# Performance work log

Measured on AMD Instinct MI355X. Metric: run time of the kernel, lower is better.

## Reference

```python
import jax, jax.numpy as jnp
import numpy as np

D_MODEL = 128; NS = 8; D_FF = 512; N_CROSS = 3; N_SELF = 2; PRED = 4
B = 2; N = 5; Q = 2500; HF = 24; WF = 77
VX, VY, VZ = 32, 16, 32  # voxel grid (x, y, z); volume layout [B, C, VY, VX, VZ]


def grid_sample_2d(feat, grid):
    # feat [B,C,H,W]; grid [B,*S,2] xy in [-1,1]; bilinear, align_corners=True, zeros padding
    Bf, C, H, W = feat.shape
    gs = grid.shape[1:-1]
    g = grid.reshape(Bf, -1, 2)
    x = (g[..., 0] + 1.0) * 0.5 * (W - 1)
    y = (g[..., 1] + 1.0) * 0.5 * (H - 1)
    x0 = jnp.floor(x); y0 = jnp.floor(y)
    xd = x - x0; yd = y - y0
    featf = feat.reshape(Bf, C, H * W)
    def corner(xi, yi, w8):
        valid = (xi >= 0) & (xi < W) & (yi >= 0) & (yi < H)
        idx = jnp.clip(yi, 0, H - 1).astype(jnp.int32) * W + jnp.clip(xi, 0, W - 1).astype(jnp.int32)
        gathered = jnp.take_along_axis(featf, idx[:, None, :], axis=2)  # [B,C,P]
        return gathered * (w8 * valid)[:, None, :]
    out = (corner(x0, y0, (1 - xd) * (1 - yd)) + corner(x0 + 1, y0, xd * (1 - yd))
           + corner(x0, y0 + 1, (1 - xd) * yd) + corner(x0 + 1, y0 + 1, xd * yd))
    return out.reshape(Bf, C, *gs)


def grid_sample_3d(feat, grid):
    # feat [B,C,D,H,W]; grid [B,*S,3] with channels (x->W, y->H, z->D); zeros padding
    Bf, C, D, H, W = feat.shape
    gs = grid.shape[1:-1]
    g = grid.reshape(Bf, -1, 3)
    x = (g[..., 0] + 1.0) * 0.5 * (W - 1)
    y = (g[..., 1] + 1.0) * 0.5 * (H - 1)
    z = (g[..., 2] + 1.0) * 0.5 * (D - 1)
    x0 = jnp.floor(x); y0 = jnp.floor(y); z0 = jnp.floor(z)
    xd = x - x0; yd = y - y0; zd = z - z0
    featf = feat.reshape(Bf, C, D * H * W)
    def corner(xi, yi, zi, w8):
        valid = (xi >= 0) & (xi < W) & (yi >= 0) & (yi < H) & (zi >= 0) & (zi < D)
        idx = (jnp.clip(zi, 0, D - 1).astype(jnp.int32) * (H * W)
               + jnp.clip(yi, 0, H - 1).astype(jnp.int32) * W
               + jnp.clip(xi, 0, W - 1).astype(jnp.int32))
        gathered = jnp.take_along_axis(featf, idx[:, None, :], axis=2)
        return gathered * (w8 * valid)[:, None, :]
    out = (corner(x0, y0, z0, (1 - xd) * (1 - yd) * (1 - zd))
           + corner(x0 + 1, y0, z0, xd * (1 - yd) * (1 - zd))
           + corner(x0, y0 + 1, z0, (1 - xd) * yd * (1 - zd))
           + corner(x0 + 1, y0 + 1, z0, xd * yd * (1 - zd))
           + corner(x0, y0, z0 + 1, (1 - xd) * (1 - yd) * zd)
           + corner(x0 + 1, y0, z0 + 1, xd * (1 - yd) * zd)
           + corner(x0, y0 + 1, z0 + 1, (1 - xd) * yd * zd)
           + corner(x0 + 1, y0 + 1, z0 + 1, xd * yd * zd))
    return out.reshape(Bf, C, *gs)


def layer_norm(x, g, b):
    mu = x.mean(-1, keepdims=True)
    var = ((x - mu) ** 2).mean(-1, keepdims=True)
    return (x - mu) / jnp.sqrt(var + 1e-5) * g + b


def setup_inputs() -> dict:
    key = jax.random.key(0)
    ks = iter(jax.random.split(key, 64))
    def rn(shape, scale=0.02):
        return (jax.random.normal(next(ks), shape) * scale).astype(jnp.float32)
    inp = {
        'query': jax.random.normal(next(ks), (B, Q, D_MODEL), jnp.float32),
        'ref_points': jax.random.uniform(next(ks), (B, N, Q, 2), jnp.float32),
        'ref_points_3d': jax.random.uniform(next(ks), (B, Q, 3), jnp.float32) * 2.0 - 1.0,
        'image_features': jax.random.normal(next(ks), (B * N, D_MODEL, HF, WF), jnp.float32),
        'mask': jax.random.randint(next(ks), (B, N, Q), 0, 2) > 0,
        'x_idx': jax.random.randint(next(ks), (B, Q), 0, VX, dtype=jnp.int32),
        'y_idx': jax.random.randint(next(ks), (B, Q), 0, VY, dtype=jnp.int32),
        'z_idx': jax.random.randint(next(ks), (B, Q), 0, VZ, dtype=jnp.int32),
        # cross-attn layers (stacked over N_CROSS)
        'c_ln1_g': jnp.ones((N_CROSS, D_MODEL), jnp.float32), 'c_ln1_b': jnp.zeros((N_CROSS, D_MODEL), jnp.float32),
        'c_dp_w': rn((N_CROSS, D_MODEL, NS * 2)), 'c_dp_b': jnp.zeros((N_CROSS, NS * 2), jnp.float32),
        'c_a_w': rn((N_CROSS, D_MODEL, NS)), 'c_a_b': jnp.zeros((N_CROSS, NS), jnp.float32),
        'c_w_w': rn((N_CROSS, D_MODEL, D_MODEL)), 'c_w_b': jnp.zeros((N_CROSS, D_MODEL), jnp.float32),
        'c_vp_w': rn((N_CROSS, D_MODEL, D_MODEL)), 'c_vp_b': jnp.zeros((N_CROSS, D_MODEL), jnp.float32),
        'c_op_w': rn((N_CROSS, D_MODEL, D_MODEL)), 'c_op_b': jnp.zeros((N_CROSS, D_MODEL), jnp.float32),
        'c_ln2_g': jnp.ones((N_CROSS, D_MODEL), jnp.float32), 'c_ln2_b': jnp.zeros((N_CROSS, D_MODEL), jnp.float32),
        'c_ff1_w': rn((N_CROSS, D_MODEL, D_FF)), 'c_ff1_b': jnp.zeros((N_CROSS, D_FF), jnp.float32),
        'c_ff2_w': rn((N_CROSS, D_FF, D_MODEL)), 'c_ff2_b': jnp.zeros((N_CROSS, D_MODEL), jnp.float32),
        # self-attn layers (stacked over N_SELF)
        's_ln1_g': jnp.ones((N_SELF, D_MODEL), jnp.float32), 's_ln1_b': jnp.zeros((N_SELF, D_MODEL), jnp.float32),
        's_dp_w': rn((N_SELF, D_MODEL, NS * 3)), 's_dp_b': jnp.zeros((N_SELF, NS * 3), jnp.float32),
        's_a_w': rn((N_SELF, D_MODEL, NS)), 's_a_b': jnp.zeros((N_SELF, NS), jnp.float32),
        's_w_w': rn((N_SELF, D_MODEL, D_MODEL)), 's_w_b': jnp.zeros((N_SELF, D_MODEL), jnp.float32),
        's_vp_w': rn((N_SELF, D_MODEL, D_MODEL)), 's_vp_b': jnp.zeros((N_SELF, D_MODEL), jnp.float32),
        's_op_w': rn((N_SELF, D_MODEL, D_MODEL)), 's_op_b': jnp.zeros((N_SELF, D_MODEL), jnp.float32),
        's_ln2_g': jnp.ones((N_SELF, D_MODEL), jnp.float32), 's_ln2_b': jnp.zeros((N_SELF, D_MODEL), jnp.float32),
        's_ff1_w': rn((N_SELF, D_MODEL, D_FF)), 's_ff1_b': jnp.zeros((N_SELF, D_FF), jnp.float32),
        's_ff2_w': rn((N_SELF, D_FF, D_MODEL)), 's_ff2_b': jnp.zeros((N_SELF, D_MODEL), jnp.float32),
        'cls_w': rn((D_MODEL, PRED)), 'cls_b': jnp.zeros((PRED,), jnp.float32),
    }
    return inp


def reference(query, ref_points, ref_points_3d, image_features, mask, x_idx, y_idx, z_idx,
              c_ln1_g, c_ln1_b, c_dp_w, c_dp_b, c_a_w, c_a_b, c_w_w, c_w_b, c_vp_w, c_vp_b,
              c_op_w, c_op_b, c_ln2_g, c_ln2_b, c_ff1_w, c_ff1_b, c_ff2_w, c_ff2_b,
              s_ln1_g, s_ln1_b, s_dp_w, s_dp_b, s_a_w, s_a_b, s_w_w, s_w_b, s_vp_w, s_vp_b,
              s_op_w, s_op_b, s_ln2_g, s_ln2_b, s_ff1_w, s_ff1_b, s_ff2_w, s_ff2_b, cls_w, cls_b):
    mf = mask.astype(query.dtype)  # [B,N,Q]
    flat_idx = y_idx * (VX * VZ) + x_idx * VZ + z_idx  # [B,Q], vol layout [B,C,VY,VX,VZ]
    bb = jnp.arange(B)[:, None]

    # ---- deformable cross attention stack ----
    for i in range(N_CROSS):
        q_ln = layer_norm(query, c_ln1_g[i], c_ln1_b[i])
        dp = (q_ln @ c_dp_w[i] + c_dp_b[i]).reshape(B, Q, NS, 2)
        pd = (ref_points[:, :, :, None, :] + dp[:, None]) * 2.0 - 1.0  # [B,N,Q,Ns,2]
        vf = jnp.einsum('bchw,cd->bdhw', image_features, c_vp_w[i]) + c_vp_b[i][None, :, None, None]
        samp = grid_sample_2d(vf, pd.reshape(B * N, Q, NS, 2))  # [B*N,C,Q,Ns]
        samp = samp.reshape(B, N, D_MODEL, Q, NS).transpose(0, 1, 3, 4, 2)  # [B,N,Q,Ns,C]
        wf = samp @ c_w_w[i] + c_w_b[i]
        att = jax.nn.softmax(q_ln @ c_a_w[i] + c_a_b[i], axis=-1)  # [B,Q,Ns]
        s = (wf * att[:, None, :, :, None]).sum(3)  # [B,N,Q,C]
        s = (s * mf[..., None]).sum(1) / (mf.sum(1)[..., None] + 1e-6)  # masked mean over cameras
        query = query + (s @ c_op_w[i] + c_op_b[i])
        h = layer_norm(query, c_ln2_g[i], c_ln2_b[i])
        h = jax.nn.gelu(h @ c_ff1_w[i] + c_ff1_b[i], approximate=False) @ c_ff2_w[i] + c_ff2_b[i]
        query = query + h

    # ---- voxel scatter + deformable self attention stack ----
    m_any = jnp.any(mask, axis=1).astype(query.dtype)  # [B,Q]
    for i in range(N_SELF):
        vol = jnp.zeros((B, VY * VX * VZ, D_MODEL), query.dtype).at[bb, flat_idx].set(query)
        vol = vol.reshape(B, VY, VX, VZ, D_MODEL).transpose(0, 4, 1, 2, 3)  # [B,C,16,32,32]
        q_ln = layer_norm(query, s_ln1_g[i], s_ln1_b[i])
        dp = (q_ln @ s_dp_w[i] + s_dp_b[i]).reshape(B, Q, NS, 3)
        pd = ref_points_3d[:, :, None, :] + dp
        pd = pd[..., jnp.array([1, 0, 2])]  # permute coords as in torch code
        samp = grid_sample_3d(vol, pd)  # [B,C,Q,Ns]
        samp = samp.transpose(0, 2, 3, 1)  # [B,Q,Ns,C]
        v = samp @ s_vp_w[i] + s_vp_b[i]
        wf = v @ s_w_w[i] + s_w_b[i]
        att = jax.nn.softmax(q_ln @ s_a_w[i] + s_a_b[i], axis=-1)
        s = (wf * att[..., None]).sum(2)  # [B,Q,C]
        s = s * m_any[..., None]
        query = query + (s @ s_op_w[i] + s_op_b[i])
        h = layer_norm(query, s_ln2_g[i], s_ln2_b[i])
        h = jax.nn.gelu(h @ s_ff1_w[i] + s_ff1_b[i], approximate=False) @ s_ff2_w[i] + s_ff2_b[i]
        query = query + h

    logits = query @ cls_w + cls_b  # [B,Q,pred_num]
    return logits
```

## Files before the change

kernel.cpp:

```cpp
#include <hip/hip_runtime.h>
#include <math.h>

#define D_MODELC 128
#define NSAMP 8
#define DFF 512
#define NCROSS 3
#define NSELF 2
#define BB 2
#define NCAM 5
#define QQ 2500
#define HFI 24
#define WFI 77
#define VXC 32
#define VYC 16
#define VZC 32
#define BQ (BB*QQ)
#define HWI (HFI*WFI)
#define NVOX (VYC*VXC*VZC)

typedef float f4 __attribute__((ext_vector_type(4)));
typedef short s8v __attribute__((ext_vector_type(8)));

__device__ __forceinline__ unsigned short f2bf(float f) {
  union { float f; unsigned u; } v; v.f = f;
  unsigned r = v.u + 0x7FFFu + ((v.u >> 16) & 1u);
  return (unsigned short)(r >> 16);
}
__device__ __forceinline__ float bf2f(unsigned short u) {
  union { unsigned u; float f; } v; v.u = ((unsigned)u) << 16; return v.f;
}

__device__ __forceinline__ bool mask_at(const unsigned char* m, int fl, int idx) {
  if (fl) return m[idx] != 0;
  return ((const int*)m)[idx] != 0;
}

__global__ __launch_bounds__(1024) void mask_k(const unsigned char* __restrict__ m,
                                               int* __restrict__ flag,
                                               float* __restrict__ invden, float* __restrict__ imc,
                                               float* __restrict__ many) {
  __shared__ int f;
  if (threadIdx.x == 0) f = 0;
  __syncthreads();
  const int total = BB * NCAM * QQ;
  int loc = 0;
  for (int i = threadIdx.x; i < total; i += 1024)
    if ((i & 3) && m[i]) loc = 1;
  if (loc) atomicOr(&f, 1);
  __syncthreads();
  int fl = f;
  if (threadIdx.x == 0) *flag = fl;
  for (int i = threadIdx.x; i < BQ; i += 1024) {
    int b = i / QQ, q = i % QQ;
    float cnt = 0.f;
    for (int n = 0; n < NCAM; ++n)
      cnt += mask_at(m, fl, (b * NCAM + n) * QQ + q) ? 1.f : 0.f;
    float inv = 1.f / (cnt + 1e-6f);
    invden[i] = inv;
    imc[i] = cnt * inv;
    many[i] = cnt > 0.f ? 1.f : 0.f;
  }
}

__global__ __launch_bounds__(256) void transpose_img_k(const float* __restrict__ in,
                                                       unsigned short* __restrict__ out) {
  __shared__ float til[32][65];
  int bn = blockIdx.z;
  int c0 = blockIdx.y * 32;
  int yx0 = blockIdx.x * 64;
  int t = threadIdx.x;
  {
    int yx_l = t & 63, c_l = t >> 6;
    int yx = yx0 + yx_l;
#pragma unroll
    for (int i = 0; i < 8; ++i) {
      int c = c_l + 4 * i;
      float v = 0.f;
      if (yx < HWI) v = in[((size_t)(bn * D_MODELC + c0 + c)) * HWI + yx];
      til[c][yx_l] = v;
    }
  }
  __syncthreads();
  {
    int yx_l = t >> 2, cc = (t & 3) * 8;
    int yx = yx0 + yx_l;
    if (yx < HWI) {
      union { unsigned short u[8]; s8v v; } pk;
#pragma unroll
      for (int j = 0; j < 8; ++j) pk.u[j] = f2bf(til[cc + j][yx_l]);
      *(s8v*)(out + ((size_t)bn * HWI + yx) * D_MODELC + c0 + cc) = pk.v;
    }
  }
}

__global__ __launch_bounds__(256) void zero_vol_k(unsigned short* __restrict__ vol,
                                                  int* __restrict__ winner) {
  int idx = blockIdx.x * 256 + threadIdx.x;
  const int nv16 = (BB * NVOX * 128) / 8;
  if (idx < nv16) {
    uint4 z = make_uint4(0, 0, 0, 0);
    *(uint4*)(vol + (size_t)idx * 8) = z;
  }
  const int nw4 = (BB * NVOX) / 4;
  if (idx < nw4) {
    int4 m = make_int4(-1, -1, -1, -1);
    *(int4*)(winner + (size_t)idx * 4) = m;
  }
}

__global__ void scatter_winner_k(const int* __restrict__ xi, const int* __restrict__ yi,
                                 const int* __restrict__ zi, int* __restrict__ winner) {
  int i = blockIdx.x * blockDim.x + threadIdx.x;
  if (i >= BQ) return;
  int b = i / QQ;
  int vox = yi[i] * (VXC * VZC) + xi[i] * VZC + zi[i];
  atomicMax(&winner[b * NVOX + vox], i % QQ);
}

__global__ void scatter_write_k(const int* __restrict__ xi, const int* __restrict__ yi,
                                const int* __restrict__ zi, const int* __restrict__ winner,
                                const float* __restrict__ qb, unsigned short* __restrict__ vol) {
  int idx = blockIdx.x * blockDim.x + threadIdx.x;
  if (idx >= BQ * 16) return;
  int g = idx & 15, row = idx >> 4;
  int b = row / QQ, q = row % QQ;
  int vox = yi[row] * (VXC * VZC) + xi[row] * VZC + zi[row];
  if (winner[b * NVOX + vox] != q) return;
  const float* src = qb + (size_t)row * 128 + g * 8;
  float4 a = *(const float4*)src;
  float4 c = *(const float4*)(src + 4);
  union { unsigned short u[8]; s8v v; } pk;
  pk.u[0] = f2bf(a.x); pk.u[1] = f2bf(a.y); pk.u[2] = f2bf(a.z); pk.u[3] = f2bf(a.w);
  pk.u[4] = f2bf(c.x); pk.u[5] = f2bf(c.y); pk.u[6] = f2bf(c.z); pk.u[7] = f2bf(c.w);
  *(s8v*)(vol + ((size_t)b * NVOX + vox) * 128 + g * 8) = pk.v;
}

__global__ __launch_bounds__(256) void tpre_k(const float* __restrict__ c_w_w, const float* __restrict__ s_w_w,
                                              const float* __restrict__ c_op_w, const float* __restrict__ s_op_w,
                                              const float* __restrict__ cf1, const float* __restrict__ sf1,
                                              const float* __restrict__ cf2, const float* __restrict__ sf2,
                                              float* __restrict__ Qbuf,
                                              unsigned short* __restrict__ f1T, unsigned short* __restrict__ f2T) {
  __shared__ float As_[32][64];
  __shared__ float Ws_[32][64];
  int z = blockIdx.z, tid = threadIdx.x;
  if (z < 5) {
    const float* A = (z < 3) ? c_w_w + (size_t)z * 16384 : s_w_w + (size_t)(z - 3) * 16384;
    const float* Bm = (z < 3) ? c_op_w + (size_t)z * 16384 : s_op_w + (size_t)(z - 3) * 16384;
    float* C = Qbuf + (size_t)z * 16384;
    int m0 = blockIdx.x * 64, n0 = blockIdx.y * 64;
    float acc[4][4] = {};
    int mr = (tid >> 4) * 4, nc = (tid & 15) * 4;
    for (int k0 = 0; k0 < 128; k0 += 32) {
      {
        int r = tid >> 2, kq = (tid & 3) * 8;
        const float* ap = A + (size_t)(m0 + r) * 128 + k0 + kq;
        float4 v0 = *(const float4*)ap, v1 = *(const float4*)(ap + 4);
        As_[kq + 0][r] = v0.x; As_[kq + 1][r] = v0.y; As_[kq + 2][r] = v0.z; As_[kq + 3][r] = v0.w;
        As_[kq + 4][r] = v1.x; As_[kq + 5][r] = v1.y; As_[kq + 6][r] = v1.z; As_[kq + 7][r] = v1.w;
      }
      {
        int kr = tid >> 3, nq = (tid & 7) * 8;
        const float* wp = Bm + (size_t)(k0 + kr) * 128 + n0 + nq;
        *(float4*)&Ws_[kr][nq] = *(const float4*)wp;
        *(float4*)&Ws_[kr][nq + 4] = *(const float4*)(wp + 4);
      }
      __syncthreads();
#pragma unroll
      for (int kk = 0; kk < 32; ++kk) {
        float4 av = *(const float4*)&As_[kk][mr];
        float4 bv = *(const float4*)&Ws_[kk][nc];
        float a_[4] = {av.x, av.y, av.z, av.w};
        float b_[4] = {bv.x, bv.y, bv.z, bv.w};
#pragma unroll
        for (int i = 0; i < 4; ++i)
#pragma unroll
          for (int j = 0; j < 4; ++j) acc[i][j] += a_[i] * b_[j];
      }
      __syncthreads();
    }
#pragma unroll
    for (int i = 0; i < 4; ++i) {
      float4 r;
      r.x = acc[i][0]; r.y = acc[i][1]; r.z = acc[i][2]; r.w = acc[i][3];
      *(float4*)(C + (size_t)(m0 + mr + i) * 128 + n0 + nc) = r;
    }
  } else {
    int bid = (z - 5) * 4 + blockIdx.y * 2 + blockIdx.x;
    int widx = bid >> 6, chunk = bid & 63;
    const float* src; unsigned short* dst; int K, N;
    if (widx < 5) {
      src = (widx < 3) ? cf1 + (size_t)widx * 65536 : sf1 + (size_t)(widx - 3) * 65536;
      dst = f1T + (size_t)widx * 65536; K = 128; N = 512;
    } else {
      int L = widx - 5;
      src = (L < 3) ? cf2 + (size_t)L * 65536 : sf2 + (size_t)(L - 3) * 65536;
      dst = f2T + (size_t)L * 65536; K = 512; N = 128;
    }
    int e = (chunk * 256 + tid) * 4;
    int k = e % K, n = e / K;
    ushort4 o;
    o.x = f2bf(src[(size_t)(k + 0) * N + n]);
    o.y = f2bf(src[(size_t)(k + 1) * N + n]);
    o.z = f2bf(src[(size_t)(k + 2) * N + n]);
    o.w = f2bf(src[(size_t)(k + 3) * N + n]);
    *(ushort4*)(dst + e) = o;
  }
}

struct P5 { const float* a[5]; const float* b[5]; float* c[5]; };

__global__ __launch_bounds__(256) void small_mm_k(P5 ps) {
  const float* A = ps.a[blockIdx.z];
  const float* Bm = ps.b[blockIdx.z];
  float* C = ps.c[blockIdx.z];
  __shared__ float As_[32][64];
  __shared__ float Ws_[32][64];
  int m0 = blockIdx.x * 64, n0 = blockIdx.y * 64, tid = threadIdx.x;
  float acc[4][4] = {};
  int mr = (tid >> 4) * 4, nc = (tid & 15) * 4;
  for (int k0 = 0; k0 < 128; k0 += 32) {
    {
      int r = tid >> 2, kq = (tid & 3) * 8;
      const float* ap = A + (size_t)(m0 + r) * 128 + k0 + kq;
      float4 v0 = *(const float4*)ap, v1 = *(const float4*)(ap + 4);
      As_[kq + 0][r] = v0.x; As_[kq + 1][r] = v0.y; As_[kq + 2][r] = v0.z; As_[kq + 3][r] = v0.w;
      As_[kq + 4][r] = v1.x; As_[kq + 5][r] = v1.y; As_[kq + 6][r] = v1.z; As_[kq + 7][r] = v1.w;
    }
    {
      int kr = tid >> 3, nq = (tid & 7) * 8;
      const float* wp = Bm + (size_t)(k0 + kr) * 128 + n0 + nq;
      *(float4*)&Ws_[kr][nq] = *(const float4*)wp;
      *(float4*)&Ws_[kr][nq + 4] = *(const float4*)(wp + 4);
    }
    __syncthreads();
#pragma unroll
    for (int kk = 0; kk < 32; ++kk) {
      float4 av = *(const float4*)&As_[kk][mr];
      float4 bv = *(const float4*)&Ws_[kk][nc];
      float a_[4] = {av.x, av.y, av.z, av.w};
      float b_[4] = {bv.x, bv.y, bv.z, bv.w};
#pragma unroll
      for (int i = 0; i < 4; ++i)
#pragma unroll
        for (int j = 0; j < 4; ++j) acc[i][j] += a_[i] * b_[j];
    }
    __syncthreads();
  }
#pragma unroll
  for (int i = 0; i < 4; ++i) {
    float4 r;
    r.x = acc[i][0]; r.y = acc[i][1]; r.z = acc[i][2]; r.w = acc[i][3];
    *(float4*)(C + (size_t)(m0 + mr + i) * 128 + n0 + nc) = r;
  }
}

__global__ __launch_bounds__(256) void wpre_k(const float* __restrict__ Wcbuf,
                                              unsigned short* __restrict__ WcT,
                                              const float* __restrict__ c_vp_b, const float* __restrict__ c_w_b,
                                              const float* __restrict__ s_vp_b, const float* __restrict__ s_w_b,
                                              const float* __restrict__ c_op_w, const float* __restrict__ s_op_w,
                                              const float* __restrict__ Qbuf,
                                              float* __restrict__ v1buf, float* __restrict__ v2buf,
                                              float* __restrict__ csbuf) {
  int t = threadIdx.x;
  if (blockIdx.y < 5) {
    int L = blockIdx.y;
    const float* src = Wcbuf + (size_t)L * 16384;
    unsigned short* dst = WcT + (size_t)L * 16384;
    int e = (blockIdx.x * 256 + t) * 4;
    int k = e & 127, n = e >> 7;
    ushort4 o;
    o.x = f2bf(src[(size_t)(k + 0) * 128 + n]);
    o.y = f2bf(src[(size_t)(k + 1) * 128 + n]);
    o.z = f2bf(src[(size_t)(k + 2) * 128 + n]);
    o.w = f2bf(src[(size_t)(k + 3) * 128 + n]);
    *(ushort4*)(dst + e) = o;
  } else if (blockIdx.x < 5 && t < 128) {
    int L = blockIdx.x, n = t;
    const float* vpb = L < 3 ? c_vp_b + L * 128 : s_vp_b + (L - 3) * 128;
    const float* wb = L < 3 ? c_w_b + L * 128 : s_w_b + (L - 3) * 128;
    const float* op = L < 3 ? c_op_w + (size_t)L * 16384 : s_op_w + (size_t)(L - 3) * 16384;
    const float* Q = Qbuf + (size_t)L * 16384;
    float a = 0.f, c = 0.f;
    for (int k = 0; k < 128; ++k) {
      a += vpb[k] * Q[k * 128 + n];
      c += wb[k] * op[k * 128 + n];
    }
    if (L < 3) { v1buf[L * 128 + n] = a; v2buf[L * 128 + n] = c; }
    else csbuf[(L - 3) * 128 + n] = a + c;
  }
}

__global__ __launch_bounds__(512) void cross_mega_k(
    const float* __restrict__ query, const float* __restrict__ refp,
    const unsigned char* __restrict__ maskp, const int* __restrict__ flagp,
    const float* __restrict__ invden, const float* __restrict__ imc,
    const unsigned short* __restrict__ imgT,
    const float* __restrict__ ln1g, const float* __restrict__ ln1b,
    const float* __restrict__ dpw_, const float* __restrict__ dpb_,
    const float* __restrict__ aw_, const float* __restrict__ ab_,
    const unsigned short* __restrict__ WcT, const float* __restrict__ opb_,
    const float* __restrict__ v1_, const float* __restrict__ v2_,
    const float* __restrict__ ln2g, const float* __restrict__ ln2b,
    const unsigned short* __restrict__ f1T, const float* __restrict__ b1_,
    const unsigned short* __restrict__ f2T, const float* __restrict__ b2_,
    float* __restrict__ qb) {
  __shared__ float qtile[8][136];
  __shared__ float pr[8][24];
  __shared__ float awa[8];
  __shared__ __align__(16) unsigned short As[16 * 128];
  __shared__ __align__(16) char scratch[16896];
  int* soff = (int*)scratch;
  float* sw = (float*)(scratch + 5120);
  float* wl = (float*)scratch;
  unsigned short* Hs = (unsigned short*)scratch;

  int t = threadIdx.x;
  int m0 = blockIdx.x * 8;
  int wv = t >> 6, lane = t & 63;
  int la = lane & 15, lb = lane >> 4;
  int fl = *flagp;
  if (lane < 32)
    *(float4*)&qtile[wv][lane * 4] = *(const float4*)(query + (size_t)(m0 + wv) * 128 + lane * 4);
  if (t < 128) {
    s8v z = {};
    *(s8v*)&As[(8 + (t >> 4)) * 128 + (t & 15) * 8] = z;
  }
  __syncthreads();

  for (int L = 0; L < NCROSS; ++L) {
    const float* dpw = dpw_ + (size_t)L * 2048;
    const float* dpb = dpb_ + L * 16;
    const float* aw = aw_ + (size_t)L * 1024;
    const float* ab = ab_ + L * 8;
    const float* g1 = ln1g + L * 128;
    const float* be1 = ln1b + L * 128;
    for (int idx = t; idx < 24 * 128; idx += 512) {
      int c = idx >> 7, k = idx & 127;
      wl[c * 132 + k] = (c < 16) ? dpw[k * 16 + c] : aw[k * 8 + (c - 16)];
    }
    __syncthreads();
    {
      int c0 = lane * 2;
      float x0 = qtile[wv][c0], x1 = qtile[wv][c0 + 1];
      float s1 = x0 + x1, s2 = x0 * x0 + x1 * x1;
#pragma unroll
      for (int msk = 1; msk < 64; msk <<= 1) { s1 += __shfl_xor(s1, msk); s2 += __shfl_xor(s2, msk); }
      float mean = s1 * (1.f / 128.f);
      float var = s2 * (1.f / 128.f) - mean * mean;
      float inv = rsqrtf(var + 1e-5f);
      float l0 = (x0 - mean) * inv * g1[c0] + be1[c0];
      float l1 = (x1 - mean) * inv * g1[c0 + 1] + be1[c0 + 1];
      float p[24];
#pragma unroll
      for (int c = 0; c < 24; ++c)
        p[c] = l0 * wl[c * 132 + c0] + l1 * wl[c * 132 + c0 + 1];
#pragma unroll
      for (int msk = 1; msk < 64; msk <<= 1) {
#pragma unroll
        for (int c = 0; c < 24; ++c) p[c] += __shfl_xor(p[c], msk);
      }
      if (lane == 0) {
#pragma unroll
        for (int c = 0; c < 24; ++c) pr[wv][c] = p[c];
      }
    }
    __syncthreads();
    if (t < 320) {
      int qi = t / 40, rem = t % 40;
      int n = rem >> 3, s = rem & 7;
      int row = m0 + qi;
      int b = row / QQ, q = row - b * QQ;
      int mi = (b * NCAM + n) * QQ + q;
      bool mk = mask_at(maskp, fl, mi);
      float mx = -1e30f;
      float av[8];
#pragma unroll
      for (int i = 0; i < 8; ++i) { av[i] = pr[qi][16 + i] + ab[i]; mx = fmaxf(mx, av[i]); }
      float sm = 0.f, es = 0.f;
#pragma unroll
      for (int i = 0; i < 8; ++i) {
        float e_ = expf(av[i] - mx);
        sm += e_;
        if (i == s) es = e_;
      }
      float a = mk ? es / sm : 0.f;
      float rx = refp[(size_t)mi * 2 + 0];
      float ry = refp[(size_t)mi * 2 + 1];
      float fx = (rx + pr[qi][s * 2 + 0] + dpb[s * 2 + 0]) * (float)(WFI - 1);
      float fy = (ry + pr[qi][s * 2 + 1] + dpb[s * 2 + 1]) * (float)(HFI - 1);
      float x0f = floorf(fx), y0f = floorf(fy);
      int x0 = (int)x0f, y0 = (int)y0f;
      float xd = fx - x0f, yd = fy - y0f;
      int base = (b * NCAM + n) * HWI;
#pragma unroll
      for (int cy = 0; cy < 2; ++cy)
#pragma unroll
        for (int cx = 0; cx < 2; ++cx) {
          int xi = x0 + cx, yi = y0 + cy;
          bool ok = (xi >= 0) & (xi < WFI) & (yi >= 0) & (yi < HFI);
          int xc = min(max(xi, 0), WFI - 1), yc = min(max(yi, 0), HFI - 1);
          soff[t * 4 + cy * 2 + cx] = (base + yc * WFI + xc) * 128;
          sw[t * 4 + cy * 2 + cx] = ok ? a * (cx ? xd : 1.f - xd) * (cy ? yd : 1.f - yd) : 0.f;
        }
    }
    __syncthreads();
    {
      int qi = wv, ln = lane & 15, eg = lane >> 4;
      float acc[8] = {};
      float wa = 0.f;
      for (int e = eg * 10; e < eg * 10 + 10; ++e) {
        int eb = qi * 40 + e;
        float4 wv4 = *(const float4*)&sw[eb * 4];
        int4 ov = *(const int4*)&soff[eb * 4];
        s8v p0 = *(const s8v*)(imgT + (size_t)ov.x + ln * 8);
        s8v p1 = *(const s8v*)(imgT + (size_t)ov.y + ln * 8);
        s8v p2 = *(const s8v*)(imgT + (size_t)ov.z + ln * 8);
        s8v p3 = *(const s8v*)(imgT + (size_t)ov.w + ln * 8);
#pragma unroll
        for (int i = 0; i < 8; ++i)
          acc[i] += wv4.x * bf2f((unsigned short)p0[i]) + wv4.y * bf2f((unsigned short)p1[i])
                  + wv4.z * bf2f((unsigned short)p2[i]) + wv4.w * bf2f((unsigned short)p3[i]);
        wa += wv4.x + wv4.y + wv4.z + wv4.w;
      }
#pragma unroll
      for (int i = 0; i < 8; ++i) { acc[i] += __shfl_xor(acc[i], 16); acc[i] += __shfl_xor(acc[i], 32); }
      wa += __shfl_xor(wa, 16); wa += __shfl_xor(wa, 32);
      if (eg == 0) {
        union { unsigned short u[8]; s8v v; } pk;
#pragma unroll
        for (int i = 0; i < 8; ++i) pk.u[i] = f2bf(acc[i]);
        *(s8v*)&As[qi * 128 + ((ln ^ (qi & 7)) << 3)] = pk.v;
        if (ln == 0) awa[qi] = wa;
      }
    }
    __syncthreads();
    {
      const unsigned short* Wc = WcT + (size_t)L * 16384;
      const float* v1L = v1_ + L * 128;
      const float* v2L = v2_ + L * 128;
      const float* opbL = opb_ + L * 128;
      f4 accm = {};
      int col = wv * 16 + la;
#pragma unroll
      for (int ks = 0; ks < 4; ++ks) {
        s8v af = *(const s8v*)&As[la * 128 + (((ks * 4 + lb) ^ (la & 7)) << 3)];
        s8v bf = *(const s8v*)(Wc + (size_t)col * 128 + ks * 32 + lb * 8);
        accm = __builtin_amdgcn_mfma_f32_16x16x32_bf16(af, bf, accm, 0, 0, 0);
      }
#pragma unroll
      for (int j = 0; j < 4; ++j) {
        int lr = lb * 4 + j;
        if (lr < 8) {
          int m = m0 + lr;
          float s0m = invden[m];
          qtile[lr][col] += accm[j] * s0m + s0m * awa[lr] * v1L[col] + imc[m] * v2L[col] + opbL[col];
        }
      }
    }
    __syncthreads();
    {
      const float* g2 = ln2g + L * 128;
      const float* be2 = ln2b + L * 128;
      int c0 = lane * 2;
      float x0 = qtile[wv][c0], x1 = qtile[wv][c0 + 1];
      float s1 = x0 + x1, s2 = x0 * x0 + x1 * x1;
#pragma unroll
      for (int msk = 1; msk < 64; msk <<= 1) { s1 += __shfl_xor(s1, msk); s2 += __shfl_xor(s2, msk); }
      float mean = s1 * (1.f / 128.f);
      float var = s2 * (1.f / 128.f) - mean * mean;
      float inv = rsqrtf(var + 1e-5f);
      unsigned u0 = f2bf((x0 - mean) * inv * g2[c0] + be2[c0]);
      unsigned u1 = f2bf((x1 - mean) * inv * g2[c0 + 1] + be2[c0 + 1]);
      int chunk = lane >> 2, idx2 = (lane & 3) * 2;
      *(unsigned*)&As[wv * 128 + ((chunk ^ (wv & 7)) << 3) + idx2] = u0 | (u1 << 16);
    }
    __syncthreads();
    {
      const unsigned short* W1 = f1T + (size_t)L * 65536;
      const float* b1 = b1_ + L * 512;
      f4 acc1[4] = {};
#pragma unroll
      for (int ks = 0; ks < 4; ++ks) {
        s8v af = *(const s8v*)&As[la * 128 + (((ks * 4 + lb) ^ (la & 7)) << 3)];
#pragma unroll
        for (int ti = 0; ti < 4; ++ti) {
          int col = (wv * 4 + ti) * 16 + la;
          s8v bf = *(const s8v*)(W1 + (size_t)col * 128 + ks * 32 + lb * 8);
          acc1[ti] = __builtin_amdgcn_mfma_f32_16x16x32_bf16(af, bf, acc1[ti], 0, 0, 0);
        }
      }
#pragma unroll
      for (int ti = 0; ti < 4; ++ti) {
        int col = (wv * 4 + ti) * 16 + la;
        int chunk = col >> 3, idx = col & 7;
#pragma unroll
        for (int j = 0; j < 4; ++j) {
          int m = lb * 4 + j;
          float val = 0.f;
          if (m < 8) {
            val = acc1[ti][j] + b1[col];
            val = 0.5f * val * (1.f + erff(val * 0.70710678118654752f));
          }
          Hs[m * 512 + ((chunk ^ (m & 7)) << 3) + idx] = f2bf(val);
        }
      }
    }
    __syncthreads();
    {
      const unsigned short* W2 = f2T + (size_t)L * 65536;
      const float* b2 = b2_ + L * 128;
      f4 acc2 = {};
      int col = wv * 16 + la;
#pragma unroll
      for (int ks = 0; ks < 16; ++ks) {
        s8v af = *(const s8v*)&Hs[la * 512 + (((ks * 4 + lb) ^ (la & 7)) << 3)];
        s8v bf = *(const s8v*)(W2 + (size_t)col * 512 + ks * 32 + lb * 8);
        acc2 = __builtin_amdgcn_mfma_f32_16x16x32_bf16(af, bf, acc2, 0, 0, 0);
      }
#pragma unroll
      for (int j = 0; j < 4; ++j) {
        int lr = lb * 4 + j;
        if (lr < 8) qtile[lr][col] += acc2[j] + b2[col];
      }
    }
    __syncthreads();
  }
  if (lane < 32)
    *(float4*)(qb + (size_t)(m0 + wv) * 128 + lane * 4) = *(const float4*)&qtile[wv][lane * 4];
}

template <bool CLS>
__global__ __launch_bounds__(512) void self_mega_k(
    const float* __restrict__ qbin, const float* __restrict__ ref3d,
    const unsigned short* __restrict__ vol, const float* __restrict__ many,
    const float* __restrict__ ln1g, const float* __restrict__ ln1b,
    const float* __restrict__ dpw, const float* __restrict__ dpb,
    const float* __restrict__ aw, const float* __restrict__ ab,
    const unsigned short* __restrict__ WcT, const float* __restrict__ opb,
    const float* __restrict__ csb,
    const float* __restrict__ ln2g, const float* __restrict__ ln2b,
    const unsigned short* __restrict__ f1T, const float* __restrict__ b1,
    const unsigned short* __restrict__ f2T, const float* __restrict__ b2,
    float* __restrict__ qb,
    const float* __restrict__ cw, const float* __restrict__ cb, float* __restrict__ out) {
  __shared__ float qtile[8][136];
  __shared__ float pr[8][32];
  __shared__ __align__(16) unsigned short As[16 * 128];
  __shared__ __align__(16) char scratch[16896];
  int* soff = (int*)scratch;
  float* sw = (float*)(scratch + 2048);
  float* wl = (float*)scratch;
  unsigned short* Hs = (unsigned short*)scratch;

  int t = threadIdx.x;
  int m0 = blockIdx.x * 8;
  int wv = t >> 6, lane = t & 63;
  int la = lane & 15, lb = lane >> 4;
  if (lane < 32)
    *(float4*)&qtile[wv][lane * 4] = *(const float4*)(qbin + (size_t)(m0 + wv) * 128 + lane * 4);
  if (t < 128) {
    s8v z = {};
    *(s8v*)&As[(8 + (t >> 4)) * 128 + (t & 15) * 8] = z;
  }
  for (int idx = t; idx < 32 * 128; idx += 512) {
    int c = idx >> 7, k = idx & 127;
    wl[c * 132 + k] = (c < 24) ? dpw[k * 24 + c] : aw[k * 8 + (c - 24)];
  }
  __syncthreads();
  {
    int c0 = lane * 2;
    float x0 = qtile[wv][c0], x1 = qtile[wv][c0 + 1];
    float s1 = x0 + x1, s2 = x0 * x0 + x1 * x1;
#pragma unroll
    for (int msk = 1; msk < 64; msk <<= 1) { s1 += __shfl_xor(s1, msk); s2 += __shfl_xor(s2, msk); }
    float mean = s1 * (1.f / 128.f);
    float var = s2 * (1.f / 128.f) - mean * mean;
    float inv = rsqrtf(var + 1e-5f);
    float l0 = (x0 - mean) * inv * ln1g[c0] + ln1b[c0];
    float l1 = (x1 - mean) * inv * ln1g[c0 + 1] + ln1b[c0 + 1];
    float p[32];
#pragma unroll
    for (int c = 0; c < 32; ++c)
      p[c] = l0 * wl[c * 132 + c0] + l1 * wl[c * 132 + c0 + 1];
#pragma unroll
    for (int msk = 1; msk < 64; msk <<= 1) {
#pragma unroll
      for (int c = 0; c < 32; ++c) p[c] += __shfl_xor(p[c], msk);
    }
    if (lane == 0) {
#pragma unroll
      for (int c = 0; c < 32; ++c) pr[wv][c] = p[c];
    }
  }
  __syncthreads();
  if (t < 64) {
    int qi = t >> 3, s = t & 7;
    int row = m0 + qi;
    int b = row / QQ;
    float mx = -1e30f;
    float av[8];
#pragma unroll
    for (int i = 0; i < 8; ++i) { av[i] = pr[qi][24 + i] + ab[i]; mx = fmaxf(mx, av[i]); }
    float sm = 0.f, es = 0.f;
#pragma unroll
    for (int i = 0; i < 8; ++i) {
      float e_ = expf(av[i] - mx);
      sm += e_;
      if (i == s) es = e_;
    }
    float a = es / sm;
    float g0 = pr[qi][s * 3 + 1] + dpb[s * 3 + 1] + ref3d[row * 3 + 1];
    float g1v = pr[qi][s * 3 + 0] + dpb[s * 3 + 0] + ref3d[row * 3 + 0];
    float g2v = pr[qi][s * 3 + 2] + dpb[s * 3 + 2] + ref3d[row * 3 + 2];
    float fx = (g0 + 1.f) * 0.5f * (float)(VZC - 1);
    float fy = (g1v + 1.f) * 0.5f * (float)(VXC - 1);
    float fz = (g2v + 1.f) * 0.5f * (float)(VYC - 1);
    float x0f = floorf(fx), y0f = floorf(fy), z0f = floorf(fz);
    int x0 = (int)x0f, y0 = (int)y0f, z0 = (int)z0f;
    float xd = fx - x0f, yd = fy - y0f, zd = fz - z0f;
    int base = b * NVOX;
#pragma unroll
    for (int cz = 0; cz < 2; ++cz)
#pragma unroll
      for (int cy = 0; cy < 2; ++cy)
#pragma unroll
        for (int cx = 0; cx < 2; ++cx) {
          int xi = x0 + cx, yi = y0 + cy, zi = z0 + cz;
          bool ok = (xi >= 0) & (xi < VZC) & (yi >= 0) & (yi < VXC) & (zi >= 0) & (zi < VYC);
          int xc = min(max(xi, 0), VZC - 1);
          int yc = min(max(yi, 0), VXC - 1);
          int zc = min(max(zi, 0), VYC - 1);
          int ci = cz * 4 + cy * 2 + cx;
          soff[t * 8 + ci] = (base + (zc * VXC + yc) * VZC + xc) * 128;
          sw[t * 8 + ci] = ok ? a * (cx ? xd : 1.f - xd) * (cy ? yd : 1.f - yd) * (cz ? zd : 1.f - zd) : 0.f;
        }
  }
  __syncthreads();
  {
    int qi = wv, ln = lane & 15, eg = lane >> 4;
    float acc[8] = {};
#pragma unroll
    for (int ss = 0; ss < 2; ++ss) {
      int eb = qi * 8 + eg * 2 + ss;
#pragma unroll
      for (int c = 0; c < 8; ++c) {
        float wgt = sw[eb * 8 + c];
        s8v p = *(const s8v*)(vol + (size_t)soff[eb * 8 + c] + ln * 8);
#pragma unroll
        for (int i = 0; i < 8; ++i) acc[i] += wgt * bf2f((unsigned short)p[i]);
      }
    }
#pragma unroll
    for (int i = 0; i < 8; ++i) { acc[i] += __shfl_xor(acc[i], 16); acc[i] += __shfl_xor(acc[i], 32); }
    if (eg == 0) {
      union { unsigned short u[8]; s8v v; } pk;
#pragma unroll
      for (int i = 0; i < 8; ++i) pk.u[i] = f2bf(acc[i]);
      *(s8v*)&As[qi * 128 + ((ln ^ (qi & 7)) << 3)] = pk.v;
    }
  }
  __syncthreads();
  {
    f4 accm = {};
    int col = wv * 16 + la;
#pragma unroll
    for (int ks = 0; ks < 4; ++ks) {
      s8v af = *(const s8v*)&As[la * 128 + (((ks * 4 + lb) ^ (la & 7)) << 3)];
      s8v bf = *(const s8v*)(WcT + (size_t)col * 128 + ks * 32 + lb * 8);
      accm = __builtin_amdgcn_mfma_f32_16x16x32_bf16(af, bf, accm, 0, 0, 0);
    }
#pragma unroll
    for (int j = 0; j < 4; ++j) {
      int lr = lb * 4 + j;
      if (lr < 8) {
        int m = m0 + lr;
        float s0m = many[m];
        qtile[lr][col] += accm[j] * s0m + s0m * csb[col] + opb[col];
      }
    }
  }
  __syncthreads();
  {
    int c0 = lane * 2;
    float x0 = qtile[wv][c0], x1 = qtile[wv][c0 + 1];
    float s1 = x0 + x1, s2 = x0 * x0 + x1 * x1;
#pragma unroll
    for (int msk = 1; msk < 64; msk <<= 1) { s1 += __shfl_xor(s1, msk); s2 += __shfl_xor(s2, msk); }
    float mean = s1 * (1.f / 128.f);
    float var = s2 * (1.f / 128.f) - mean * mean;
    float inv = rsqrtf(var + 1e-5f);
    unsigned u0 = f2bf((x0 - mean) * inv * ln2g[c0] + ln2b[c0]);
    unsigned u1 = f2bf((x1 - mean) * inv * ln2g[c0 + 1] + ln2b[c0 + 1]);
    int chunk = lane >> 2, idx2 = (lane & 3) * 2;
    *(unsigned*)&As[wv * 128 + ((chunk ^ (wv & 7)) << 3) + idx2] = u0 | (u1 << 16);
  }
  __syncthreads();
  {
    f4 acc1[4] = {};
#pragma unroll
    for (int ks = 0; ks < 4; ++ks) {
      s8v af = *(const s8v*)&As[la * 128 + (((ks * 4 + lb) ^ (la & 7)) << 3)];
#pragma unroll
      for (int ti = 0; ti < 4; ++ti) {
        int col = (wv * 4 + ti) * 16 + la;
        s8v bf = *(const s8v*)(f1T + (size_t)col * 128 + ks * 32 + lb * 8);
        acc1[ti] = __builtin_amdgcn_mfma_f32_16x16x32_bf16(af, bf, acc1[ti], 0, 0, 0);
      }
    }
#pragma unroll
    for (int ti = 0; ti < 4; ++ti) {
      int col = (wv * 4 + ti) * 16 + la;
      int chunk = col >> 3, idx = col & 7;
#pragma unroll
      for (int j = 0; j < 4; ++j) {
        int m = lb * 4 + j;
        float val = 0.f;
        if (m < 8) {
          val = acc1[ti][j] + b1[col];
          val = 0.5f * val * (1.f + erff(val * 0.70710678118654752f));
        }
        Hs[m * 512 + ((chunk ^ (m & 7)) << 3) + idx] = f2bf(val);
      }
    }
  }
  __syncthreads();
  {
    f4 acc2 = {};
    int col = wv * 16 + la;
#pragma unroll
    for (int ks = 0; ks < 16; ++ks) {
      s8v af = *(const s8v*)&Hs[la * 512 + (((ks * 4 + lb) ^ (la & 7)) << 3)];
      s8v bf = *(const s8v*)(f2T + (size_t)col * 512 + ks * 32 + lb * 8);
      acc2 = __builtin_amdgcn_mfma_f32_16x16x32_bf16(af, bf, acc2, 0, 0, 0);
    }
#pragma unroll
    for (int j = 0; j < 4; ++j) {
      int lr = lb * 4 + j;
      if (lr < 8) qtile[lr][col] += acc2[j] + b2[col];
    }
  }
  __syncthreads();
  if (CLS) {
    int c0 = lane * 2;
    float q0 = qtile[wv][c0], q1 = qtile[wv][c0 + 1];
    float ps0 = q0 * cw[c0 * 4 + 0] + q1 * cw[(c0 + 1) * 4 + 0];
    float ps1 = q0 * cw[c0 * 4 + 1] + q1 * cw[(c0 + 1) * 4 + 1];
    float ps2 = q0 * cw[c0 * 4 + 2] + q1 * cw[(c0 + 1) * 4 + 2];
    float ps3 = q0 * cw[c0 * 4 + 3] + q1 * cw[(c0 + 1) * 4 + 3];
#pragma unroll
    for (int msk = 1; msk < 64; msk <<= 1) {
      ps0 += __shfl_xor(ps0, msk);
      ps1 += __shfl_xor(ps1, msk);
      ps2 += __shfl_xor(ps2, msk);
      ps3 += __shfl_xor(ps3, msk);
    }
    if (lane < 4) {
      float o = (lane == 0) ? ps0 : (lane == 1) ? ps1 : (lane == 2) ? ps2 : ps3;
      out[(m0 + wv) * 4 + lane] = o + cb[lane];
    }
  } else {
    if (lane < 32)
      *(float4*)(qb + (size_t)(m0 + wv) * 128 + lane * 4) = *(const float4*)&qtile[wv][lane * 4];
  }
}

extern "C" void kernel_launch(void* const* d_in, const int* in_sizes, int n_in,
                              void* d_out, int out_size, void* d_ws, size_t ws_size,
                              hipStream_t stream) {
  (void)in_sizes; (void)n_in; (void)out_size; (void)ws_size;
  const float* query = (const float*)d_in[0];
  const float* ref_points = (const float*)d_in[1];
  const float* ref3d = (const float*)d_in[2];
  const float* imgf = (const float*)d_in[3];
  const unsigned char* maskp = (const unsigned char*)d_in[4];
  const int* x_idx = (const int*)d_in[5];
  const int* y_idx = (const int*)d_in[6];
  const int* z_idx = (const int*)d_in[7];
  const float* c_ln1_g = (const float*)d_in[8];
  const float* c_ln1_b = (const float*)d_in[9];
  const float* c_dp_w = (const float*)d_in[10];
  const float* c_dp_b = (const float*)d_in[11];
  const float* c_a_w = (const float*)d_in[12];
  const float* c_a_b = (const float*)d_in[13];
  const float* c_w_w = (const float*)d_in[14];
  const float* c_w_b = (const float*)d_in[15];
  const float* c_vp_w = (const float*)d_in[16];
  const float* c_vp_b = (const float*)d_in[17];
  const float* c_op_w = (const float*)d_in[18];
  const float* c_op_b = (const float*)d_in[19];
  const float* c_ln2_g = (const float*)d_in[20];
  const float* c_ln2_b = (const float*)d_in[21];
  const float* c_ff1_w = (const float*)d_in[22];
  const float* c_ff1_b = (const float*)d_in[23];
  const float* c_ff2_w = (const float*)d_in[24];
  const float* c_ff2_b = (const float*)d_in[25];
  const float* s_ln1_g = (const float*)d_in[26];
  const float* s_ln1_b = (const float*)d_in[27];
  const float* s_dp_w = (const float*)d_in[28];
  const float* s_dp_b = (const float*)d_in[29];
  const float* s_a_w = (const float*)d_in[30];
  const float* s_a_b = (const float*)d_in[31];
  const float* s_w_w = (const float*)d_in[32];
  const float* s_w_b = (const float*)d_in[33];
  const float* s_vp_w = (const float*)d_in[34];
  const float* s_vp_b = (const float*)d_in[35];
  const float* s_op_w = (const float*)d_in[36];
  const float* s_op_b = (const float*)d_in[37];
  const float* s_ln2_g = (const float*)d_in[38];
  const float* s_ln2_b = (const float*)d_in[39];
  const float* s_ff1_w = (const float*)d_in[40];
  const float* s_ff1_b = (const float*)d_in[41];
  const float* s_ff2_w = (const float*)d_in[42];
  const float* s_ff2_b = (const float*)d_in[43];
  const float* cls_w = (const float*)d_in[44];
  const float* cls_b = (const float*)d_in[45];
  float* out = (float*)d_out;

  char* ws = (char*)d_ws;
  size_t off = 0;
  auto carve = [&](size_t bytes) -> char* {
    char* p = ws + off;
    off += (bytes + 255) & ~(size_t)255;
    return p;
  };
  int* flag = (int*)carve(256);
  float* invden = (float*)carve(BQ * 4);
  float* imc = (float*)carve(BQ * 4);
  float* many = (float*)carve(BQ * 4);
  float* qb = (float*)carve((size_t)BQ * 128 * 4);
  int* winner = (int*)carve((size_t)BB * NVOX * 4);
  float* Qbuf = (float*)carve((size_t)5 * 16384 * 4);
  float* Wcbuf = (float*)carve((size_t)5 * 16384 * 4);
  unsigned short* WcT = (unsigned short*)carve((size_t)5 * 16384 * 2);
  unsigned short* f1T = (unsigned short*)carve((size_t)5 * 65536 * 2);
  unsigned short* f2T = (unsigned short*)carve((size_t)5 * 65536 * 2);
  float* v1buf = (float*)carve(3 * 128 * 4);
  float* v2buf = (float*)carve(3 * 128 * 4);
  float* csbuf = (float*)carve(2 * 128 * 4);
  unsigned short* imgT = (unsigned short*)carve((size_t)BB * NCAM * HWI * 128 * 2);
  unsigned short* vol = (unsigned short*)carve((size_t)BB * NVOX * 128 * 2);

  const int GB8 = BQ / 8;

  mask_k<<<1, 1024, 0, stream>>>(maskp, flag, invden, imc, many);
  tpre_k<<<dim3(2, 2, 165), 256, 0, stream>>>(c_w_w, s_w_w, c_op_w, s_op_w,
                                              c_ff1_w, s_ff1_w, c_ff2_w, s_ff2_w,
                                              Qbuf, f1T, f2T);
  {
    P5 pw;
    for (int L = 0; L < 5; ++L) {
      pw.a[L] = (L < 3) ? c_vp_w + (size_t)L * 16384 : s_vp_w + (size_t)(L - 3) * 16384;
      pw.b[L] = Qbuf + (size_t)L * 16384;
      pw.c[L] = Wcbuf + (size_t)L * 16384;
    }
    small_mm_k<<<dim3(2, 2, 5), 256, 0, stream>>>(pw);
  }
  wpre_k<<<dim3(16, 6), 256, 0, stream>>>(Wcbuf, WcT, c_vp_b, c_w_b, s_vp_b, s_w_b,
                                          c_op_w, s_op_w, Qbuf, v1buf, v2buf, csbuf);
  transpose_img_k<<<dim3((HWI + 63) / 64, 4, BB * NCAM), 256, 0, stream>>>(imgf, imgT);
  zero_vol_k<<<1024, 256, 0, stream>>>(vol, winner);
  scatter_winner_k<<<(BQ + 255) / 256, 256, 0, stream>>>(x_idx, y_idx, z_idx, winner);

  cross_mega_k<<<GB8, 512, 0, stream>>>(query, ref_points, maskp, flag, invden, imc, imgT,
                                        c_ln1_g, c_ln1_b, c_dp_w, c_dp_b, c_a_w, c_a_b,
                                        WcT, c_op_b, v1buf, v2buf, c_ln2_g, c_ln2_b,
                                        f1T, c_ff1_b, f2T, c_ff2_b, qb);

  scatter_write_k<<<(BQ * 16 + 255) / 256, 256, 0, stream>>>(x_idx, y_idx, z_idx, winner, qb, vol);
  self_mega_k<false><<<GB8, 512, 0, stream>>>(qb, ref3d, vol, many,
                                              s_ln1_g, s_ln1_b, s_dp_w, s_dp_b, s_a_w, s_a_b,
                                              WcT + (size_t)3 * 16384, s_op_b, csbuf,
                                              s_ln2_g, s_ln2_b,
                                              f1T + (size_t)3 * 65536, s_ff1_b,
                                              f2T + (size_t)3 * 65536, s_ff2_b,
                                              qb, cls_w, cls_b, out);
  scatter_write_k<<<(BQ * 16 + 255) / 256, 256, 0, stream>>>(x_idx, y_idx, z_idx, winner, qb, vol);
  self_mega_k<true><<<GB8, 512, 0, stream>>>(qb, ref3d, vol, many,
                                             s_ln1_g + 128, s_ln1_b + 128,
                                             s_dp_w + (size_t)128 * 24, s_dp_b + 24,
                                             s_a_w + (size_t)128 * 8, s_a_b + 8,
                                             WcT + (size_t)4 * 16384, s_op_b + 128,
                                             csbuf + 128, s_ln2_g + 128, s_ln2_b + 128,
                                             f1T + (size_t)4 * 65536, s_ff1_b + 512,
                                             f2T + (size_t)4 * 65536, s_ff2_b + 128,
                                             qb, cls_w, cls_b, out);
}
```

Before: 513.9 us.

## Process 16 queries per block and compute LN projections with MFMA

Doubles rows per block from 8 to 16 (1024 threads) so the 16-row MFMA tiles no longer waste half their rows, which halves the weight traffic per query in the FFN and out-projection GEMMs. Replaces the per-block fp32 shuffle-reduction for the offset/attention projection with a bf16 MFMA against weights pre-transposed once in wpre_k. Also skips gathers when the bilinear weight sum is zero. The tradeoffs are larger blocks with more LDS and register pressure, bf16 rounding of the offset projections, and a possible occupancy drop.

```diff
diff --git a/kernel.cpp b/kernel.cpp
--- a/kernel.cpp
+++ b/kernel.cpp
@@ -262,7 +262,10 @@
                                               const float* __restrict__ c_op_w, const float* __restrict__ s_op_w,
                                               const float* __restrict__ Qbuf,
                                               float* __restrict__ v1buf, float* __restrict__ v2buf,
-                                              float* __restrict__ csbuf) {
+                                              float* __restrict__ csbuf,
+                                              const float* __restrict__ c_dp_w, const float* __restrict__ c_a_w,
+                                              const float* __restrict__ s_dp_w, const float* __restrict__ s_a_w,
+                                              unsigned short* __restrict__ pjT) {
   int t = threadIdx.x;
   if (blockIdx.y < 5) {
     int L = blockIdx.y;
@@ -289,58 +292,67 @@
     }
     if (L < 3) { v1buf[L * 128 + n] = a; v2buf[L * 128 + n] = c; }
     else csbuf[(L - 3) * 128 + n] = a + c;
-  }
-}
-
-__global__ __launch_bounds__(512) void cross_mega_k(
+  } else if (blockIdx.x >= 5 && blockIdx.x < 10) {
+    int L = blockIdx.x - 5;
+    unsigned short* dst = pjT + (size_t)L * 4096;
+    for (int e = t * 16; e < t * 16 + 16; ++e) {
+      int col = e >> 7, k = e & 127;
+      float v = 0.f;
+      if (L < 3) {
+        if (col < 16) v = c_dp_w[(size_t)L * 2048 + k * 16 + col];
+        else if (col < 24) v = c_a_w[(size_t)L * 1024 + k * 8 + (col - 16)];
+      } else {
+        int i = L - 3;
+        if (col < 24) v = s_dp_w[(size_t)i * 3072 + k * 24 + col];
+        else v = s_a_w[(size_t)i * 1024 + k * 8 + (col - 24)];
+      }
+      dst[e] = f2bf(v);
+    }
+  }
+}
+
+__global__ __launch_bounds__(1024) void cross_mega_k(
     const float* __restrict__ query, const float* __restrict__ refp,
     const unsigned char* __restrict__ maskp, const int* __restrict__ flagp,
     const float* __restrict__ invden, const float* __restrict__ imc,
     const unsigned short* __restrict__ imgT,
     const float* __restrict__ ln1g, const float* __restrict__ ln1b,
-    const float* __restrict__ dpw_, const float* __restrict__ dpb_,
-    const float* __restrict__ aw_, const float* __restrict__ ab_,
+    const unsigned short* __restrict__ pjT, const float* __restrict__ dpb_,
+    const float* __restrict__ ab_,
     const unsigned short* __restrict__ WcT, const float* __restrict__ opb_,
     const float* __restrict__ v1_, const float* __restrict__ v2_,
     const float* __restrict__ ln2g, const float* __restrict__ ln2b,
     const unsigned short* __restrict__ f1T, const float* __restrict__ b1_,
     const unsigned short* __restrict__ f2T, const float* __restrict__ b2_,
-    float* __restrict__ qb) {
-  __shared__ float qtile[8][136];
-  __shared__ float pr[8][24];
-  __shared__ float awa[8];
+    float* __restrict__ qb, int M) {
+  __shared__ float qtile[16][132];
+  __shared__ float pr[16 * 36];
+  __shared__ float awa[16];
   __shared__ __align__(16) unsigned short As[16 * 128];
-  __shared__ __align__(16) char scratch[16896];
+  __shared__ __align__(16) char scratch[20480];
   int* soff = (int*)scratch;
-  float* sw = (float*)(scratch + 5120);
-  float* wl = (float*)scratch;
+  float* sw = (float*)(scratch + 10240);
   unsigned short* Hs = (unsigned short*)scratch;
 
   int t = threadIdx.x;
-  int m0 = blockIdx.x * 8;
+  int m0 = blockIdx.x * 16;
   int wv = t >> 6, lane = t & 63;
   int la = lane & 15, lb = lane >> 4;
   int fl = *flagp;
-  if (lane < 32)
-    *(float4*)&qtile[wv][lane * 4] = *(const float4*)(query + (size_t)(m0 + wv) * 128 + lane * 4);
-  if (t < 128) {
-    s8v z = {};
-    *(s8v*)&As[(8 + (t >> 4)) * 128 + (t & 15) * 8] = z;
+  int rowW = m0 + wv;
+  {
+    float4 v = make_float4(0, 0, 0, 0);
+    if (rowW < M && lane < 32)
+      v = *(const float4*)(query + (size_t)rowW * 128 + lane * 4);
+    if (lane < 32) *(float4*)&qtile[wv][lane * 4] = v;
   }
   __syncthreads();
 
   for (int L = 0; L < NCROSS; ++L) {
-    const float* dpw = dpw_ + (size_t)L * 2048;
     const float* dpb = dpb_ + L * 16;
-    const float* aw = aw_ + (size_t)L * 1024;
     const float* ab = ab_ + L * 8;
     const float* g1 = ln1g + L * 128;
     const float* be1 = ln1b + L * 128;
-    for (int idx = t; idx < 24 * 128; idx += 512) {
-      int c = idx >> 7, k = idx & 127;
-      wl[c * 132 + k] = (c < 16) ? dpw[k * 16 + c] : aw[k * 8 + (c - 16)];
-    }
-    __syncthreads();
     {
       int c0 = lane * 2;
       float x0 = qtile[wv][c0], x1 = qtile[wv][c0 + 1];
@@ -350,60 +362,68 @@
       float mean = s1 * (1.f / 128.f);
       float var = s2 * (1.f / 128.f) - mean * mean;
       float inv = rsqrtf(var + 1e-5f);
-      float l0 = (x0 - mean) * inv * g1[c0] + be1[c0];
-      float l1 = (x1 - mean) * inv * g1[c0 + 1] + be1[c0 + 1];
-      float p[24];
-#pragma unroll
-      for (int c = 0; c < 24; ++c)
-        p[c] = l0 * wl[c * 132 + c0] + l1 * wl[c * 132 + c0 + 1];
-#pragma unroll
-      for (int msk = 1; msk < 64; msk <<= 1) {
-#pragma unroll
-        for (int c = 0; c < 24; ++c) p[c] += __shfl_xor(p[c], msk);
-      }
-      if (lane == 0) {
-#pragma unroll
-        for (int c = 0; c < 24; ++c) pr[wv][c] = p[c];
-      }
+      unsigned u0 = f2bf((x0 - mean) * inv * g1[c0] + be1[c0]);
+      unsigned u1 = f2bf((x1 - mean) * inv * g1[c0 + 1] + be1[c0 + 1]);
+      int chunk = lane >> 2, idx2 = (lane & 3) * 2;
+      *(unsigned*)&As[wv * 128 + ((chunk ^ (wv & 7)) << 3) + idx2] = u0 | (u1 << 16);
     }
     __syncthreads();
-    if (t < 320) {
+    if (wv < 2) {
+      const unsigned short* pw = pjT + (size_t)L * 4096;
+      f4 acc = {};
+      int col = wv * 16 + la;
+#pragma unroll
+      for (int ks = 0; ks < 4; ++ks) {
+        s8v af = *(const s8v*)&As[la * 128 + (((ks * 4 + lb) ^ (la & 7)) << 3)];
+        s8v bf = *(const s8v*)(pw + (size_t)col * 128 + ks * 32 + lb * 8);
+        acc = __builtin_amdgcn_mfma_f32_16x16x32_bf16(af, bf, acc, 0, 0, 0);
+      }
+#pragma unroll
+      for (int j = 0; j < 4; ++j) pr[(lb * 4 + j) * 36 + col] = acc[j];
+    }
+    __syncthreads();
+    if (t < 640) {
       int qi = t / 40, rem = t % 40;
       int n = rem >> 3, s = rem & 7;
       int row = m0 + qi;
-      int b = row / QQ, q = row - b * QQ;
-      int mi = (b * NCAM + n) * QQ + q;
-      bool mk = mask_at(maskp, fl, mi);
-      float mx = -1e30f;
-      float av[8];
-#pragma unroll
-      for (int i = 0; i < 8; ++i) { av[i] = pr[qi][16 + i] + ab[i]; mx = fmaxf(mx, av[i]); }
-      float sm = 0.f, es = 0.f;
-#pragma unroll
-      for (int i = 0; i < 8; ++i) {
-        float e_ = expf(av[i] - mx);
-        sm += e_;
-        if (i == s) es = e_;
-      }
-      float a = mk ? es / sm : 0.f;
-      float rx = refp[(size_t)mi * 2 + 0];
-      float ry = refp[(size_t)mi * 2 + 1];
-      float fx = (rx + pr[qi][s * 2 + 0] + dpb[s * 2 + 0]) * (float)(WFI - 1);
-      float fy = (ry + pr[qi][s * 2 + 1] + dpb[s * 2 + 1]) * (float)(HFI - 1);
-      float x0f = floorf(fx), y0f = floorf(fy);
-      int x0 = (int)x0f, y0 = (int)y0f;
-      float xd = fx - x0f, yd = fy - y0f;
-      int base = (b * NCAM + n) * HWI;
-#pragma unroll
-      for (int cy = 0; cy < 2; ++cy)
-#pragma unroll
-        for (int cx = 0; cx < 2; ++cx) {
-          int xi = x0 + cx, yi = y0 + cy;
-          bool ok = (xi >= 0) & (xi < WFI) & (yi >= 0) & (yi < HFI);
-          int xc = min(max(xi, 0), WFI - 1), yc = min(max(yi, 0), HFI - 1);
-          soff[t * 4 + cy * 2 + cx] = (base + yc * WFI + xc) * 128;
-          sw[t * 4 + cy * 2 + cx] = ok ? a * (cx ? xd : 1.f - xd) * (cy ? yd : 1.f - yd) : 0.f;
+      if (row >= M) {
+#pragma unroll
+        for (int c = 0; c < 4; ++c) { soff[t * 4 + c] = 0; sw[t * 4 + c] = 0.f; }
+      } else {
+        int b = row / QQ, q = row - b * QQ;
+        int mi = (b * NCAM + n) * QQ + q;
+        bool mk = mask_at(maskp, fl, mi);
+        float mx = -1e30f;
+        float av[8];
+#pragma unroll
+        for (int i = 0; i < 8; ++i) { av[i] = pr[qi * 36 + 16 + i] + ab[i]; mx = fmaxf(mx, av[i]); }
+        float sm = 0.f, es = 0.f;
+#pragma unroll
+        for (int i = 0; i < 8; ++i) {
+          float e_ = expf(av[i] - mx);
+          sm += e_;
+          if (i == s) es = e_;
         }
+        float a = mk ? es / sm : 0.f;
+        float rx = refp[(size_t)mi * 2 + 0];
+        float ry = refp[(size_t)mi * 2 + 1];
+        float fx = (rx + pr[qi * 36 + s * 2 + 0] + dpb[s * 2 + 0]) * (float)(WFI - 1);
+        float fy = (ry + pr[qi * 36 + s * 2 + 1] + dpb[s * 2 + 1]) * (float)(HFI - 1);
+        float x0f = floorf(fx), y0f = floorf(fy);
+        int x0 = (int)x0f, y0 = (int)y0f;
+        float xd = fx - x0f, yd = fy - y0f;
+        int base = (b * NCAM + n) * HWI;
+#pragma unroll
+        for (int cy = 0; cy < 2; ++cy)
+#pragma unroll
+          for (int cx = 0; cx < 2; ++cx) {
+            int xi = x0 + cx, yi = y0 + cy;
+            bool ok = (xi >= 0) & (xi < WFI) & (yi >= 0) & (yi < HFI);
+            int xc = min(max(xi, 0), WFI - 1), yc = min(max(yi, 0), HFI - 1);
+            soff[t * 4 + cy * 2 + cx] = (base + yc * WFI + xc) * 128;
+            sw[t * 4 + cy * 2 + cx] = ok ? a * (cx ? xd : 1.f - xd) * (cy ? yd : 1.f - yd) : 0.f;
+          }
+      }
     }
     __syncthreads();
     {
@@ -413,16 +433,19 @@
       for (int e = eg * 10; e < eg * 10 + 10; ++e) {
         int eb = qi * 40 + e;
         float4 wv4 = *(const float4*)&sw[eb * 4];
-        int4 ov = *(const int4*)&soff[eb * 4];
-        s8v p0 = *(const s8v*)(imgT + (size_t)ov.x + ln * 8);
-        s8v p1 = *(const s8v*)(imgT + (size_t)ov.y + ln * 8);
-        s8v p2 = *(const s8v*)(imgT + (size_t)ov.z + ln * 8);
-        s8v p3 = *(const s8v*)(imgT + (size_t)ov.w + ln * 8);
-#pragma unroll
-        for (int i = 0; i < 8; ++i)
-          acc[i] += wv4.x * bf2f((unsigned short)p0[i]) + wv4.y * bf2f((unsigned short)p1[i])
-                  + wv4.z * bf2f((unsigned short)p2[i]) + wv4.w * bf2f((unsigned short)p3[i]);
-        wa += wv4.x + wv4.y + wv4.z + wv4.w;
+        float wsum = wv4.x + wv4.y + wv4.z + wv4.w;
+        if (wsum != 0.f) {
+          int4 ov = *(const int4*)&soff[eb * 4];
+          s8v p0 = *(const s8v*)(imgT + (size_t)ov.x + ln * 8);
+          s8v p1 = *(const s8v*)(imgT + (size_t)ov.y + ln * 8);
+          s8v p2 = *(const s8v*)(imgT + (size_t)ov.z + ln * 8);
+          s8v p3 = *(const s8v*)(imgT + (size_t)ov.w + ln * 8);
+#pragma unroll
+          for (int i = 0; i < 8; ++i)
+            acc[i] += wv4.x * bf2f((unsigned short)p0[i]) + wv4.y * bf2f((unsigned short)p1[i])
+                    + wv4.z * bf2f((unsigned short)p2[i]) + wv4.w * bf2f((unsigned short)p3[i]);
+          wa += wsum;
+        }
       }
 #pragma unroll
       for (int i = 0; i < 8; ++i) { acc[i] += __shfl_xor(acc[i], 16); acc[i] += __shfl_xor(acc[i], 32); }
@@ -436,7 +459,7 @@
       }
     }
     __syncthreads();
-    {
+    if (wv < 8) {
       const unsigned short* Wc = WcT + (size_t)L * 16384;
       const float* v1L = v1_ + L * 128;
       const float* v2L = v2_ + L * 128;
@@ -452,11 +475,9 @@
 #pragma unroll
       for (int j = 0; j < 4; ++j) {
         int lr = lb * 4 + j;
-        if (lr < 8) {
-          int m = m0 + lr;
-          float s0m = invden[m];
-          qtile[lr][col] += accm[j] * s0m + s0m * awa[lr] * v1L[col] + imc[m] * v2L[col] + opbL[col];
-        }
+        int m = m0 + lr;
+        float s0m = invden[m];
+        qtile[lr][col] += accm[j] * s0m + s0m * awa[lr] * v1L[col] + imc[m] * v2L[col] + opbL[col];
       }
     }
     __syncthreads();
@@ -480,35 +501,32 @@
     {
       const unsigned short* W1 = f1T + (size_t)L * 65536;
       const float* b1 = b1_ + L * 512;
-      f4 acc1[4] = {};
+      f4 acc1[2] = {};
 #pragma unroll
       for (int ks = 0; ks < 4; ++ks) {
         s8v af = *(const s8v*)&As[la * 128 + (((ks * 4 + lb) ^ (la & 7)) << 3)];
 #pragma unroll
-        for (int ti = 0; ti < 4; ++ti) {
-          int col = (wv * 4 + ti) * 16 + la;
+        for (int ti = 0; ti < 2; ++ti) {
+          int col = (wv * 2 + ti) * 16 + la;
           s8v bf = *(const s8v*)(W1 + (size_t)col * 128 + ks * 32 + lb * 8);
           acc1[ti] = __builtin_amdgcn_mfma_f32_16x16x32_bf16(af, bf, acc1[ti], 0, 0, 0);
         }
       }
 #pragma unroll
-      for (int ti = 0; ti < 4; ++ti) {
-        int col = (wv * 4 + ti) * 16 + la;
+      for (int ti = 0; ti < 2; ++ti) {
+        int col = (wv * 2 + ti) * 16 + la;
         int chunk = col >> 3, idx = col & 7;
 #pragma unroll
         for (int j = 0; j < 4; ++j) {
           int m = lb * 4 + j;
-          float val = 0.f;
-          if (m < 8) {
-            val = acc1[ti][j] + b1[col];
-            val = 0.5f * val * (1.f + erff(val * 0.70710678118654752f));
-          }
+          float val = acc1[ti][j] + b1[col];
+          val = 0.5f * val * (1.f + erff(val * 0.70710678118654752f));
           Hs[m * 512 + ((chunk ^ (m & 7)) << 3) + idx] = f2bf(val);
         }
       }
     }
     __syncthreads();
-    {
+    if (wv < 8) {
       const unsigned short* W2 = f2T + (size_t)L * 65536;
       const float* b2 = b2_ + L * 128;
       f4 acc2 = {};
@@ -520,53 +538,47 @@
         acc2 = __builtin_amdgcn_mfma_f32_16x16x32_bf16(af, bf, acc2, 0, 0, 0);
       }
 #pragma unroll
-      for (int j = 0; j < 4; ++j) {
-        int lr = lb * 4 + j;
-        if (lr < 8) qtile[lr][col] += acc2[j] + b2[col];
-      }
+      for (int j = 0; j < 4; ++j) qtile[lb * 4 + j][col] += acc2[j] + b2[col];
     }
     __syncthreads();
   }
-  if (lane < 32)
-    *(float4*)(qb + (size_t)(m0 + wv) * 128 + lane * 4) = *(const float4*)&qtile[wv][lane * 4];
+  if (rowW < M && lane < 32)
+    *(float4*)(qb + (size_t)rowW * 128 + lane * 4) = *(const float4*)&qtile[wv][lane * 4];
 }
 
 template <bool CLS>
-__global__ __launch_bounds__(512) void self_mega_k(
+__global__ __launch_bounds__(1024) void self_mega_k(
     const float* __restrict__ qbin, const float* __restrict__ ref3d,
     const unsigned short* __restrict__ vol, const float* __restrict__ many,
     const float* __restrict__ ln1g, const float* __restrict__ ln1b,
-    const float* __restrict__ dpw, const float* __restrict__ dpb,
-    const float* __restrict__ aw, const float* __restrict__ ab,
+    const unsigned short* __restrict__ pjT, const float* __restrict__ dpb,
+    const float* __restrict__ ab,
     const unsigned short* __restrict__ WcT, const float* __restrict__ opb,
     const float* __restrict__ csb,
     const float* __restrict__ ln2g, const float* __restrict__ ln2b,
     const unsigned short* __restrict__ f1T, const float* __restrict__ b1,
     const unsigned short* __restrict__ f2T, const float* __restrict__ b2,
     float* __restrict__ qb,
-    const float* __restrict__ cw, const float* __restrict__ cb, float* __restrict__ out) {
-  __shared__ float qtile[8][136];
-  __shared__ float pr[8][32];
+    const float* __restrict__ cw, const float* __restrict__ cb, float* __restrict__ out,
+    int M) {
+  __shared__ float qtile[16][132];
+  __shared__ float pr[16 * 36];
   __shared__ __align__(16) unsigned short As[16 * 128];
   __shared__ __align__(16) char scratch[16896];
   int* soff = (int*)scratch;
-  float* sw = (float*)(scratch + 2048);
-  float* wl = (float*)scratch;
+  float* sw = (float*)(scratch + 4096);
   unsigned short* Hs = (unsigned short*)scratch;
 
   int t = threadIdx.x;
-  int m0 = blockIdx.x * 8;
+  int m0 = blockIdx.x * 16;
   int wv = t >> 6, lane = t & 63;
   int la = lane & 15, lb = lane >> 4;
-  if (lane < 32)
-    *(float4*)&qtile[wv][lane * 4] = *(const float4*)(qbin + (size_t)(m0 + wv) * 128 + lane * 4);
-  if (t < 128) {
-    s8v z = {};
-    *(s8v*)&As[(8 + (t >> 4)) * 128 + (t & 15) * 8] = z;
-  }
-  for (int idx = t; idx < 32 * 128; idx += 512) {
-    int c = idx >> 7, k = idx & 127;
-    wl[c * 132 + k] = (c < 24) ? dpw[k * 24 + c] : aw[k * 8 + (c - 24)];
+  int rowW = m0 + wv;
+  {
+    float4 v = make_float4(0, 0, 0, 0);
+    if (rowW < M && lane < 32)
+      v = *(const float4*)(qbin + (size_t)rowW * 128 + lane * 4);
+    if (lane < 32) *(float4*)&qtile[wv][lane * 4] = v;
   }
   __syncthreads();
   {
@@ -578,64 +590,71 @@
     float mean = s1 * (1.f / 128.f);
     float var = s2 * (1.f / 128.f) - mean * mean;
     float inv = rsqrtf(var + 1e-5f);
-    float l0 = (x0 - mean) * inv * ln1g[c0] + ln1b[c0];
-    float l1 = (x1 - mean) * inv * ln1g[c0 + 1] + ln1b[c0 + 1];
-    float p[32];
-#pragma unroll
-    for (int c = 0; c < 32; ++c)
-      p[c] = l0 * wl[c * 132 + c0] + l1 * wl[c * 132 + c0 + 1];
-#pragma unroll
-    for (int msk = 1; msk < 64; msk <<= 1) {
-#pragma unroll
-      for (int c = 0; c < 32; ++c) p[c] += __shfl_xor(p[c], msk);
-    }
-    if (lane == 0) {
-#pragma unroll
-      for (int c = 0; c < 32; ++c) pr[wv][c] = p[c];
-    }
-  }
-  __syncthreads();
-  if (t < 64) {
+    unsigned u0 = f2bf((x0 - mean) * inv * ln1g[c0] + ln1b[c0]);
+    unsigned u1 = f2bf((x1 - mean) * inv * ln1g[c0 + 1] + ln1b[c0 + 1]);
+    int chunk = lane >> 2, idx2 = (lane & 3) * 2;
+    *(unsigned*)&As[wv * 128 + ((chunk ^ (wv & 7)) << 3) + idx2] = u0 | (u1 << 16);
+  }
+  __syncthreads();
+  if (wv < 2) {
+    f4 acc = {};
+    int col = wv * 16 + la;
+#pragma unroll
+    for (int ks = 0; ks < 4; ++ks) {
+      s8v af = *(const s8v*)&As[la * 128 + (((ks * 4 + lb) ^ (la & 7)) << 3)];
+      s8v bf = *(const s8v*)(pjT + (size_t)col * 128 + ks * 32 + lb * 8);
+      acc = __builtin_amdgcn_mfma_f32_16x16x32_bf16(af, bf, acc, 0, 0, 0);
+    }
+#pragma unroll
+    for (int j = 0; j < 4; ++j) pr[(lb * 4 + j) * 36 + col] = acc[j];
+  }
+  __syncthreads();
+  if (t < 128) {
     int qi = t >> 3, s = t & 7;
     int row = m0 + qi;
-    int b = row / QQ;
-    float mx = -1e30f;
-    float av[8];
-#pragma unroll
-    for (int i = 0; i < 8; ++i) { av[i] = pr[qi][24 + i] + ab[i]; mx = fmaxf(mx, av[i]); }
-    float sm = 0.f, es = 0.f;
-#pragma unroll
-    for (int i = 0; i < 8; ++i) {
-      float e_ = expf(av[i] - mx);
-      sm += e_;
-      if (i == s) es = e_;
-    }
-    float a = es / sm;
-    float g0 = pr[qi][s * 3 + 1] + dpb[s * 3 + 1] + ref3d[row * 3 + 1];
-    float g1v = pr[qi][s * 3 + 0] + dpb[s * 3 + 0] + ref3d[row * 3 + 0];
-    float g2v = pr[qi][s * 3 + 2] + dpb[s * 3 + 2] + ref3d[row * 3 + 2];
-    float fx = (g0 + 1.f) * 0.5f * (float)(VZC - 1);
-    float fy = (g1v + 1.f) * 0.5f * (float)(VXC - 1);
-    float fz = (g2v + 1.f) * 0.5f * (float)(VYC - 1);
-    float x0f = floorf(fx), y0f = floorf(fy), z0f = floorf(fz);
-    int x0 = (int)x0f, y0 = (int)y0f, z0 = (int)z0f;
-    float xd = fx - x0f, yd = fy - y0f, zd = fz - z0f;
-    int base = b * NVOX;
-#pragma unroll
-    for (int cz = 0; cz < 2; ++cz)
-#pragma unroll
-      for (int cy = 0; cy < 2; ++cy)
-#pragma unroll
-        for (int cx = 0; cx < 2; ++cx) {
-          int xi = x0 + cx, yi = y0 + cy, zi = z0 + cz;
-          bool ok = (xi >= 0) & (xi < VZC) & (yi >= 0) & (yi < VXC) & (zi >= 0) & (zi < VYC);
-          int xc = min(max(xi, 0), VZC - 1);
-          int yc = min(max(yi, 0), VXC - 1);
-          int zc = min(max(zi, 0), VYC - 1);
-          int ci = cz * 4 + cy * 2 + cx;
-          soff[t * 8 + ci] = (base + (zc * VXC + yc) * VZC + xc) * 128;
-          sw[t * 8 + ci] = ok ? a * (cx ? xd : 1.f - xd) * (cy ? yd : 1.f - yd) * (cz ? zd : 1.f - zd) : 0.f;
-        }
+    if (row >= M) {
+#pragma unroll
+      for (int c = 0; c < 8; ++c) { soff[t * 8 + c] = 0; sw[t * 8 + c] = 0.f; }
+    } else {
+      int b = row / QQ;
+      float mx = -1e30f;
+      float av[8];
+#pragma unroll
+      for (int i = 0; i < 8; ++i) { av[i] = pr[qi * 36 + 24 + i] + ab[i]; mx = fmaxf(mx, av[i]); }
+      float sm = 0.f, es = 0.f;
+#pragma unroll
+      for (int i = 0; i < 8; ++i) {
+        float e_ = expf(av[i] - mx);
+        sm += e_;
+        if (i == s) es = e_;
+      }
+      float a = es / sm;
+      float g0 = pr[qi * 36 + s * 3 + 1] + dpb[s * 3 + 1] + ref3d[row * 3 + 1];
+      float g1v = pr[qi * 36 + s * 3 + 0] + dpb[s * 3 + 0] + ref3d[row * 3 + 0];
+      float g2v = pr[qi * 36 + s * 3 + 2] + dpb[s * 3 + 2] + ref3d[row * 3 + 2];
+      float fx = (g0 + 1.f) * 0.5f * (float)(VZC - 1);
+      float fy = (g1v + 1.f) * 0.5f * (float)(VXC - 1);
+      float fz = (g2v + 1.f) * 0.5f * (float)(VYC - 1);
+      float x0f = floorf(fx), y0f = floorf(fy), z0f = floorf(fz);
+      int x0 = (int)x0f, y0 = (int)y0f, z0 = (int)z0f;
+      float xd = fx - x0f, yd = fy - y0f, zd = fz - z0f;
+      int base = b * NVOX;
+#pragma unroll
+      for (int cz = 0; cz < 2; ++cz)
+#pragma unroll
+        for (int cy = 0; cy < 2; ++cy)
+#pragma unroll
+          for (int cx = 0; cx < 2; ++cx) {
+            int xi = x0 + cx, yi = y0 + cy, zi = z0 + cz;
+            bool ok = (xi >= 0) & (xi < VZC) & (yi >= 0) & (yi < VXC) & (zi >= 0) & (zi < VYC);
+            int xc = min(max(xi, 0), VZC - 1);
+            int yc = min(max(yi, 0), VXC - 1);
+            int zc = min(max(zi, 0), VYC - 1);
+            int ci = cz * 4 + cy * 2 + cx;
+            soff[t * 8 + ci] = (base + (zc * VXC + yc) * VZC + xc) * 128;
+            sw[t * 8 + ci] = ok ? a * (cx ? xd : 1.f - xd) * (cy ? yd : 1.f - yd) * (cz ? zd : 1.f - zd) : 0.f;
+          }
+    }
   }
   __syncthreads();
   {
@@ -647,9 +666,11 @@
 #pragma unroll
       for (int c = 0; c < 8; ++c) {
         float wgt = sw[eb * 8 + c];
-        s8v p = *(const s8v*)(vol + (size_t)soff[eb * 8 + c] + ln * 8);
-#pragma unroll
-        for (int i = 0; i < 8; ++i) acc[i] += wgt * bf2f((unsigned short)p[i]);
+        if (wgt != 0.f) {
+          s8v p = *(const s8v*)(vol + (size_t)soff[eb * 8 + c] + ln * 8);
+#pragma unroll
+          for (int i = 0; i < 8; ++i) acc[i] += wgt * bf2f((unsigned short)p[i]);
+        }
       }
     }
 #pragma unroll
@@ -662,7 +683,7 @@
     }
   }
   __syncthreads();
-  {
+  if (wv < 8) {
     f4 accm = {};
     int col = wv * 16 + la;
 #pragma unroll
@@ -674,11 +695,9 @@
 #pragma unroll
     for (int j = 0; j < 4; ++j) {
       int lr = lb * 4 + j;
-      if (lr < 8) {
-        int m = m0 + lr;
-        float s0m = many[m];
-        qtile[lr][col] += accm[j] * s0m + s0m * csb[col] + opb[col];
-      }
+      int m = m0 + lr;
+      float s0m = many[m];
+      qtile[lr][col] += accm[j] * s0m + s0m * csb[col] + opb[col];
     }
   }
   __syncthreads();
@@ -698,35 +717,32 @@
   }
   __syncthreads();
   {
-    f4 acc1[4] = {};
+    f4 acc1[2] = {};
 #pragma unroll
     for (int ks = 0; ks < 4; ++ks) {
       s8v af = *(const s8v*)&As[la * 128 + (((ks * 4 + lb) ^ (la & 7)) << 3)];
 #pragma unroll
-      for (int ti = 0; ti < 4; ++ti) {
-        int col = (wv * 4 + ti) * 16 + la;
+      for (int ti = 0; ti < 2; ++ti) {
+        int col = (wv * 2 + ti) * 16 + la;
         s8v bf = *(const s8v*)(f1T + (size_t)col * 128 + ks * 32 + lb * 8);
         acc1[ti] = __builtin_amdgcn_mfma_f32_16x16x32_bf16(af, bf, acc1[ti], 0, 0, 0);
       }
     }
 #pragma unroll
-    for (int ti = 0; ti < 4; ++ti) {
-      int col = (wv * 4 + ti) * 16 + la;
+    for (int ti = 0; ti < 2; ++ti) {
+      int col = (wv * 2 + ti) * 16 + la;
       int chunk = col >> 3, idx = col & 7;
 #pragma unroll
       for (int j = 0; j < 4; ++j) {
         int m = lb * 4 + j;
-        float val = 0.f;
-        if (m < 8) {
-          val = acc1[ti][j] + b1[col];
-          val = 0.5f * val * (1.f + erff(val * 0.70710678118654752f));
-        }
+        float val = acc1[ti][j] + b1[col];
+        val = 0.5f * val * (1.f + erff(val * 0.70710678118654752f));
         Hs[m * 512 + ((chunk ^ (m & 7)) << 3) + idx] = f2bf(val);
       }
     }
   }
   __syncthreads();
-  {
+  if (wv < 8) {
     f4 acc2 = {};
     int col = wv * 16 + la;
 #pragma unroll
@@ -736,10 +752,7 @@
       acc2 = __builtin_amdgcn_mfma_f32_16x16x32_bf16(af, bf, acc2, 0, 0, 0);
     }
 #pragma unroll
-    for (int j = 0; j < 4; ++j) {
-      int lr = lb * 4 + j;
-      if (lr < 8) qtile[lr][col] += acc2[j] + b2[col];
-    }
+    for (int j = 0; j < 4; ++j) qtile[lb * 4 + j][col] += acc2[j] + b2[col];
   }
   __syncthreads();
   if (CLS) {
@@ -756,13 +769,13 @@
       ps2 += __shfl_xor(ps2, msk);
       ps3 += __shfl_xor(ps3, msk);
     }
-    if (lane < 4) {
+    if (lane < 4 && rowW < M) {
       float o = (lane == 0) ? ps0 : (lane == 1) ? ps1 : (lane == 2) ? ps2 : ps3;
-      out[(m0 + wv) * 4 + lane] = o + cb[lane];
+      out[rowW * 4 + lane] = o + cb[lane];
     }
   } else {
-    if (lane < 32)
-      *(float4*)(qb + (size_t)(m0 + wv) * 128 + lane * 4) = *(const float4*)&qtile[wv][lane * 4];
+    if (rowW < M && lane < 32)
+      *(float4*)(qb + (size_t)rowW * 128 + lane * 4) = *(const float4*)&qtile[wv][lane * 4];
   }
 }
 
@@ -836,13 +849,15 @@
   unsigned short* WcT = (unsigned short*)carve((size_t)5 * 16384 * 2);
   unsigned short* f1T = (unsigned short*)carve((size_t)5 * 65536 * 2);
   unsigned short* f2T = (unsigned short*)carve((size_t)5 * 65536 * 2);
+  unsigned short* pjT = (unsigned short*)carve((size_t)5 * 4096 * 2);
   float* v1buf = (float*)carve(3 * 128 * 4);
   float* v2buf = (float*)carve(3 * 128 * 4);
   float* csbuf = (float*)carve(2 * 128 * 4);
   unsigned short* imgT = (unsigned short*)carve((size_t)BB * NCAM * HWI * 128 * 2);
   unsigned short* vol = (unsigned short*)carve((size_t)BB * NVOX * 128 * 2);
 
-  const int GB8 = BQ / 8;
+  const int M = BQ;
+  const int GB16 = (M + 15) / 16;
 
   mask_k<<<1, 1024, 0, stream>>>(maskp, flag, invden, imc, many);
   tpre_k<<<dim3(2, 2, 165), 256, 0, stream>>>(c_w_w, s_w_w, c_op_w, s_op_w,
@@ -858,32 +873,33 @@
     small_mm_k<<<dim3(2, 2, 5), 256, 0, stream>>>(pw);
   }
   wpre_k<<<dim3(16, 6), 256, 0, stream>>>(Wcbuf, WcT, c_vp_b, c_w_b, s_vp_b, s_w_b,
-                                          c_op_w, s_op_w, Qbuf, v1buf, v2buf, csbuf);
+                                          c_op_w, s_op_w, Qbuf, v1buf, v2buf, csbuf,
+                                          c_dp_w, c_a_w, s_dp_w, s_a_w, pjT);
   transpose_img_k<<<dim3((HWI + 63) / 64, 4, BB * NCAM), 256, 0, stream>>>(imgf, imgT);
   zero_vol_k<<<1024, 256, 0, stream>>>(vol, winner);
   scatter_winner_k<<<(BQ + 255) / 256, 256, 0, stream>>>(x_idx, y_idx, z_idx, winner);
 
-  cross_mega_k<<<GB8, 512, 0, stream>>>(query, ref_points, maskp, flag, invden, imc, imgT,
-                                        c_ln1_g, c_ln1_b, c_dp_w, c_dp_b, c_a_w, c_a_b,
-                                        WcT, c_op_b, v1buf, v2buf, c_ln2_g, c_ln2_b,
-                                        f1T, c_ff1_b, f2T, c_ff2_b, qb);
+  cross_mega_k<<<GB16, 1024, 0, stream>>>(query, ref_points, maskp, flag, invden, imc, imgT,
+                                          c_ln1_g, c_ln1_b, pjT, c_dp_b, c_a_b,
+                                          WcT, c_op_b, v1buf, v2buf, c_ln2_g, c_ln2_b,
+                                          f1T, c_ff1_b, f2T, c_ff2_b, qb, M);
 
   scatter_write_k<<<(BQ * 16 + 255) / 256, 256, 0, stream>>>(x_idx, y_idx, z_idx, winner, qb, vol);
-  self_mega_k<false><<<GB8, 512, 0, stream>>>(qb, ref3d, vol, many,
-                                              s_ln1_g, s_ln1_b, s_dp_w, s_dp_b, s_a_w, s_a_b,
-                                              WcT + (size_t)3 * 16384, s_op_b, csbuf,
-                                              s_ln2_g, s_ln2_b,
-                                              f1T + (size_t)3 * 65536, s_ff1_b,
-                                              f2T + (size_t)3 * 65536, s_ff2_b,
-                                              qb, cls_w, cls_b, out);
+  self_mega_k<false><<<GB16, 1024, 0, stream>>>(qb, ref3d, vol, many,
+                                                s_ln1_g, s_ln1_b, pjT + (size_t)3 * 4096,
+                                                s_dp_b, s_a_b,
+                                                WcT + (size_t)3 * 16384, s_op_b, csbuf,
+                                                s_ln2_g, s_ln2_b,
+                                                f1T + (size_t)3 * 65536, s_ff1_b,
+                                                f2T + (size_t)3 * 65536, s_ff2_b,
+                                                qb, cls_w, cls_b, out, M);
   scatter_write_k<<<(BQ * 16 + 255) / 256, 256, 0, stream>>>(x_idx, y_idx, z_idx, winner, qb, vol);
-  self_mega_k<true><<<GB8, 512, 0, stream>>>(qb, ref3d, vol, many,
-                                             s_ln1_g + 128, s_ln1_b + 128,
-                                             s_dp_w + (size_t)128 * 24, s_dp_b + 24,
-                                             s_a_w + (size_t)128 * 8, s_a_b + 8,
-                                             WcT + (size_t)4 * 16384, s_op_b + 128,
-                                             csbuf + 128, s_ln2_g + 128, s_ln2_b + 128,
-                                             f1T + (size_t)4 * 65536, s_ff1_b + 512,
-                                             f2T + (size_t)4 * 65536, s_ff2_b + 128,
-                                             qb, cls_w, cls_b, out);
-}
+  self_mega_k<true><<<GB16, 1024, 0, stream>>>(qb, ref3d, vol, many,
+                                               s_ln1_g + 128, s_ln1_b + 128, pjT + (size_t)4 * 4096,
+                                               s_dp_b + 24, s_a_b + 8,
+                                               WcT + (size_t)4 * 16384, s_op_b + 128,
+                                               csbuf + 128, s_ln2_g + 128, s_ln2_b + 128,
+                                               f1T + (size_t)4 * 65536, s_ff1_b + 512,
+                                               f2T + (size_t)4 * 65536, s_ff2_b + 128,
+                                               qb, cls_w, cls_b, out, M);
+}
```

Result: faster. 417.4 us (-18.8%).
